# Performance work log

Hardware: AMD Instinct MI355X
Metric: run time of the kernel (lower is better)

Reference implementation:

```python
import jax, jax.numpy as jnp
import numpy as np

K = 1024   # in_dim = out_dim = per-head dim (module uses full k per head)
H = 4      # heads
B, T = 2, 2048


def setup_inputs() -> dict:
    key = jax.random.key(0)
    ks = jax.random.split(key, 7)
    s = 0.02
    return {
        "x": jax.random.normal(ks[0], (B, T, K), jnp.float32),
        "Wq": jax.random.normal(ks[1], (K, K * H), jnp.float32) * s,
        "Wk": jax.random.normal(ks[2], (K, K * H), jnp.float32) * s,
        "Wv": jax.random.normal(ks[3], (K, K * H), jnp.float32) * s,
        "Wu": jax.random.normal(ks[4], (K * H, K), jnp.float32) * s,
        "bu": jnp.zeros((K,), jnp.float32),
        "W1": jax.random.normal(ks[5], (K, K), jnp.float32) * s,
        "b1": jnp.zeros((K,), jnp.float32),
        "W2": jax.random.normal(ks[6], (K, K), jnp.float32) * s,
        "b2": jnp.zeros((K,), jnp.float32),
    }


def reference(x, Wq, Wk, Wv, Wu, bu, W1, b1, W2, b2):
    b, t, k = x.shape
    h = H
    scale = k ** (-0.25)
    # projections: each head gets FULL dim k (quirk of the original module)
    q = (x @ Wq).reshape(b, t, h, k) * scale   # [b,t,h,k]
    kk = (x @ Wk).reshape(b, t, h, k) * scale
    v = (x @ Wv).reshape(b, t, h, k)
    # attention scores [b,h,q,k_pos]
    dot = jnp.einsum("bqhd,bkhd->bhqk", q, kk)
    causal = jnp.tril(jnp.ones((t, t), bool))  # strictly-upper masked to -inf
    dot = jnp.where(causal, dot, -jnp.inf)
    attn = jax.nn.softmax(dot, axis=-1)
    out = jnp.einsum("bhqk,bkhd->bqhd", attn, v).reshape(b, t, h * k)
    attn_out = out @ Wu + bu                   # unifyheads
    x = x + attn_out                            # residual
    ff = jax.nn.relu(x @ W1 + b1) @ W2 + b2     # in_dim == out_dim
    return x + ff                               # residual around FFN
```

## Files before the change

kernel.cpp:

```cpp
#include <hip/hip_runtime.h>
#include <math.h>


#define TM 128
#define TN 128
#define BK 64

typedef __attribute__((ext_vector_type(8))) short short8;
typedef __attribute__((ext_vector_type(4))) float f32x4;

__device__ __forceinline__ unsigned short f2bf(float f) {
  union { float f; unsigned int u; } v; v.f = f;
  unsigned int r = (v.u + 0x7fffu + ((v.u >> 16) & 1u)) >> 16;
  return (unsigned short)r;
}
__device__ __forceinline__ float bf2f(unsigned short b) {
  union { unsigned int u; float f; } v; v.u = ((unsigned int)b) << 16;
  return v.f;
}

#define GL2LDS(g, l)                                                          \
  __builtin_amdgcn_global_load_lds(                                           \
      (__attribute__((address_space(1))) void*)(g),                           \
      (__attribute__((address_space(3))) void*)(l), 16, 0, 0)

__device__ __forceinline__ void gemm_core(
    const unsigned short* __restrict__ A, const unsigned short* __restrict__ BT,
    int m0, int n0, int kmax, int lda, int ldb, int ldc, long long coff,
    float scale, const float* __restrict__ bias,
    const float* __restrict__ resid, int do_relu, float* __restrict__ Cf,
    unsigned short* __restrict__ Cb, unsigned short* As, unsigned short* Bs) {
  const int tid = threadIdx.x;
  const int lane = tid & 63;
  const int wv = tid >> 6;
  const int wm = wv & 1;
  const int wn = wv >> 1;

  const int srow = tid >> 2;
  const int scol = (tid & 3) * 8;
  const unsigned short* ap0 = A + (long long)(m0 + srow) * lda + scol;
  const unsigned short* ap1 = ap0 + (long long)64 * lda;
  const unsigned short* bp0 = BT + (long long)(n0 + srow) * ldb + scol;
  const unsigned short* bp1 = bp0 + (long long)64 * ldb;
  unsigned short* lA00 = As + wv * 512;
  unsigned short* lA10 = As + 2048 + wv * 512;
  unsigned short* lA01 = As + 4096 + wv * 512;
  unsigned short* lA11 = As + 6144 + wv * 512;
  unsigned short* lB00 = Bs + wv * 512;
  unsigned short* lB10 = Bs + 2048 + wv * 512;
  unsigned short* lB01 = Bs + 4096 + wv * 512;
  unsigned short* lB11 = Bs + 6144 + wv * 512;

  f32x4 acc[4][4];
#pragma unroll
  for (int i = 0; i < 4; ++i)
#pragma unroll
    for (int j2 = 0; j2 < 4; ++j2) acc[i][j2] = {0.f, 0.f, 0.f, 0.f};

  const int frow = lane & 15;
  const int fq = (lane >> 4) * 8;

  for (int k0 = 0; k0 < kmax; k0 += BK) {
    __syncthreads();
    GL2LDS(ap0, lA00); GL2LDS(ap0 + 32, lA01);
    GL2LDS(ap1, lA10); GL2LDS(ap1 + 32, lA11);
    GL2LDS(bp0, lB00); GL2LDS(bp0 + 32, lB01);
    GL2LDS(bp1, lB10); GL2LDS(bp1 + 32, lB11);
    ap0 += BK; ap1 += BK; bp0 += BK; bp1 += BK;
    __syncthreads();

#pragma unroll
    for (int s = 0; s < 2; ++s) {
      short8 afr[4], bfr[4];
#pragma unroll
      for (int mi = 0; mi < 4; ++mi)
        afr[mi] = *(const short8*)(As + s * 4096 +
                                   (wm * 64 + mi * 16 + frow) * 32 + fq);
#pragma unroll
      for (int ni = 0; ni < 4; ++ni)
        bfr[ni] = *(const short8*)(Bs + s * 4096 +
                                   (wn * 64 + ni * 16 + frow) * 32 + fq);
#pragma unroll
      for (int mi = 0; mi < 4; ++mi)
#pragma unroll
        for (int ni = 0; ni < 4; ++ni)
          acc[mi][ni] = __builtin_amdgcn_mfma_f32_16x16x32_bf16(
              afr[mi], bfr[ni], acc[mi][ni], 0, 0, 0);
    }
  }

  const int ccol = lane & 15;
  const int crow = (lane >> 4) * 4;
#pragma unroll
  for (int mi = 0; mi < 4; ++mi) {
#pragma unroll
    for (int ni = 0; ni < 4; ++ni) {
      const int gc = n0 + wn * 64 + ni * 16 + ccol;
#pragma unroll
      for (int r = 0; r < 4; ++r) {
        const int gr = m0 + wm * 64 + mi * 16 + crow + r;
        float v = acc[mi][ni][r] * scale;
        if (bias) v += bias[gc];
        if (resid) v += resid[(long long)gr * ldc + gc];
        if (do_relu) v = fmaxf(v, 0.f);
        const long long ci = coff + (long long)gr * ldc + gc;
        if (Cf) Cf[ci] = v;
        if (Cb) Cb[ci] = f2bf(v);
      }
    }
  }
}

__device__ __forceinline__ void core64(
    f32x4 acc[4][2], const unsigned short* __restrict__ A, int lda,
    const unsigned short* __restrict__ BT, int ldb, int kmax,
    unsigned short* As, unsigned short* Bs) {
  const int tid = threadIdx.x;
  const int lane = tid & 63;
  const int wv = tid >> 6;
  const int wm = wv & 1;
  const int wn = wv >> 1;
  const int srow = tid >> 2;
  const int scol = (tid & 3) * 8;
  const unsigned short* ap0 = A + (long long)srow * lda + scol;
  const unsigned short* ap1 = ap0 + (long long)64 * lda;
  const unsigned short* bp0 = BT + (long long)srow * ldb + scol;
  unsigned short* lA00 = As + wv * 512;
  unsigned short* lA10 = As + 2048 + wv * 512;
  unsigned short* lA01 = As + 4096 + wv * 512;
  unsigned short* lA11 = As + 6144 + wv * 512;
  unsigned short* lB00 = Bs + wv * 512;
  unsigned short* lB01 = Bs + 2048 + wv * 512;
  const int frow = lane & 15;
  const int fq = (lane >> 4) * 8;
  for (int k0 = 0; k0 < kmax; k0 += 64) {
    __syncthreads();
    GL2LDS(ap0, lA00); GL2LDS(ap0 + 32, lA01);
    GL2LDS(ap1, lA10); GL2LDS(ap1 + 32, lA11);
    GL2LDS(bp0, lB00); GL2LDS(bp0 + 32, lB01);
    ap0 += 64; ap1 += 64; bp0 += 64;
    __syncthreads();
#pragma unroll
    for (int s = 0; s < 2; ++s) {
      short8 afr[4], bfr[2];
#pragma unroll
      for (int mi = 0; mi < 4; ++mi)
        afr[mi] = *(const short8*)(As + s * 4096 +
                                   (wm * 64 + mi * 16 + frow) * 32 + fq);
#pragma unroll
      for (int ni = 0; ni < 2; ++ni)
        bfr[ni] = *(const short8*)(Bs + s * 2048 +
                                   (wn * 32 + ni * 16 + frow) * 32 + fq);
#pragma unroll
      for (int mi = 0; mi < 4; ++mi)
#pragma unroll
        for (int ni = 0; ni < 2; ++ni)
          acc[mi][ni] = __builtin_amdgcn_mfma_f32_16x16x32_bf16(
              afr[mi], bfr[ni], acc[mi][ni], 0, 0, 0);
    }
  }
}

__global__ __launch_bounds__(256) void gemm_ffn(
    const unsigned short* __restrict__ A, const unsigned short* __restrict__ BT,
    const float* __restrict__ bias, const float* __restrict__ resid,
    int do_relu, float* __restrict__ Cf, unsigned short* __restrict__ Cb) {
  __shared__ unsigned short As[8192];
  __shared__ unsigned short Bs[4096];
  const int bid = blockIdx.x;
  const int xcd = bid & 7;
  const int j = bid >> 3;
  const int m0 = (xcd * 4 + (j & 3)) * 128;
  const int n0 = (j >> 2) * 64;
  f32x4 acc[4][2];
#pragma unroll
  for (int i = 0; i < 4; ++i)
#pragma unroll
    for (int j2 = 0; j2 < 2; ++j2) acc[i][j2] = {0.f, 0.f, 0.f, 0.f};
  core64(acc, A + (long long)m0 * 1024, 1024, BT + (long long)n0 * 1024, 1024,
         1024, As, Bs);
  const int lane = threadIdx.x & 63;
  const int wv = threadIdx.x >> 6;
  const int wm = wv & 1, wn = wv >> 1;
  const int ccol = lane & 15, crow = (lane >> 4) * 4;
#pragma unroll
  for (int mi = 0; mi < 4; ++mi) {
#pragma unroll
    for (int ni = 0; ni < 2; ++ni) {
      const int gc = n0 + wn * 32 + ni * 16 + ccol;
#pragma unroll
      for (int r = 0; r < 4; ++r) {
        const int gr = m0 + wm * 64 + mi * 16 + crow + r;
        float v = acc[mi][ni][r] + bias[gc];
        if (resid) v += resid[(long long)gr * 1024 + gc];
        if (do_relu) v = fmaxf(v, 0.f);
        const long long ci = (long long)gr * 1024 + gc;
        if (Cf) Cf[ci] = v;
        if (Cb) Cb[ci] = f2bf(v);
      }
    }
  }
}

__global__ __launch_bounds__(256) void gemm_bt(
    const unsigned short* __restrict__ A, const unsigned short* __restrict__ BT,
    int Kd, int lda, int ldb, int ldc, int bh_shift,
    long long aob, long long aoh, long long bob, long long boh,
    long long cob, long long coh, float scale,
    const float* __restrict__ bias, const float* __restrict__ resid,
    int do_relu, float* __restrict__ Cf, unsigned short* __restrict__ Cb,
    int causal_mode, int grid_mode) {
  __shared__ unsigned short As[8192];
  __shared__ unsigned short Bs[8192];
  int n0, m0, z;
  if (grid_mode == 2) {
    z = blockIdx.x; n0 = blockIdx.y * TN; m0 = blockIdx.z * TM;
  } else if (grid_mode == 4) {
    z = blockIdx.x; m0 = blockIdx.y * TM; n0 = blockIdx.z * TN;
  } else {
    n0 = blockIdx.x * TN; m0 = blockIdx.y * TM; z = blockIdx.z;
  }

  const int zb = z >> bh_shift;
  const int zh = z & ((1 << bh_shift) - 1);
  const long long aoff = (long long)zb * aob + (long long)zh * aoh;
  const long long boff = (long long)zb * bob + (long long)zh * boh;
  const long long coff = (long long)zb * cob + (long long)zh * coh;

  int kmax = Kd;
  if (causal_mode == 2) { int t = m0 + TM; if (t < kmax) kmax = t; }

  gemm_core(A + aoff, BT + boff, m0, n0, kmax, lda, ldb, ldc, coff, scale,
            bias, resid, do_relu, Cf, Cb, As, Bs);
}

__global__ __launch_bounds__(256) void gemm_t(
    const unsigned short* __restrict__ xb,
    const unsigned short* __restrict__ Wcomb,
    unsigned short* __restrict__ tb) {
  __shared__ unsigned short As[8192];
  __shared__ unsigned short Bs[8192];
  const int bid = blockIdx.x;
  const int xcd = bid & 7;
  const int j = bid >> 3;
  const int m0 = (xcd * 4 + (j & 3)) * TM;
  const int n0 = (j >> 2) * TN;
  gemm_core(xb, Wcomb, m0, n0, 1024, 1024, 1024, 4096, 0, 1.0f,
            nullptr, nullptr, 0, nullptr, tb, As, Bs);
}

__global__ __launch_bounds__(256) void gemm_sv(
    const unsigned short* __restrict__ xb,
    const unsigned short* __restrict__ Wcomb,
    const unsigned short* __restrict__ tb,
    unsigned short* __restrict__ S, unsigned short* __restrict__ vT) {
  __shared__ unsigned short As[8192];
  __shared__ unsigned short Bs[8192];
  const long long TT = (long long)2048 * 2048;
  const int bid = blockIdx.x;
  if (bid < 1088) {
    const int z = bid & 7, zb = z >> 2, zh = z & 3;
    const int idx = bid >> 3;
    int m = (int)((sqrtf(8.0f * idx + 1.0f) - 1.0f) * 0.5f);
    while ((m + 1) * (m + 2) / 2 <= idx) ++m;
    while (m * (m + 1) / 2 > idx) --m;
    const int m0 = m * TM;
    const int n0 = (idx - m * (m + 1) / 2) * TN;
    gemm_core(tb + (long long)zb * 2048 * 4096 + zh * 1024,
              xb + (long long)zb * 2048 * 1024,
              m0, n0, 1024, 4096, 1024, 2048,
              (long long)zb * 4 * TT + (long long)zh * TT,
              1.0f, nullptr, nullptr, 0, nullptr, S, As, Bs);
  } else {
    const int r = bid - 1088;
    const int xcd = r & 7;
    const int j = r >> 3;
    const int bb = j >> 6;
    const int rr = j & 63;
    const int m0 = (xcd * 4 + (rr & 3)) * TM;
    const int n0 = (rr >> 2) * TN;
    gemm_core(Wcomb + (size_t)4096 * 1024, xb + (long long)bb * 2048 * 1024,
              m0, n0, 1024, 1024, 1024, 2048, (long long)bb * 4096 * 2048,
              1.0f, nullptr, nullptr, 0, nullptr, vT, As, Bs);
  }
}

__global__ __launch_bounds__(256) void reduce_epi(
    const unsigned short* __restrict__ Pb, int S, long long MN,
    const float* __restrict__ bias, const float* __restrict__ resid,
    int do_relu, float* __restrict__ Cf, unsigned short* __restrict__ Cb) {
  const long long i4 = ((long long)blockIdx.x * 256 + threadIdx.x) * 4;
  if (i4 >= MN) return;
  float4 s = {0.f, 0.f, 0.f, 0.f};
  for (int t = 0; t < S; ++t) {
    const ushort4 p = *(const ushort4*)(Pb + (long long)t * MN + i4);
    s.x += bf2f(p.x); s.y += bf2f(p.y); s.z += bf2f(p.z); s.w += bf2f(p.w);
  }
  if (bias) {
    const int c0 = (int)(i4 & 1023);
    s.x += bias[c0]; s.y += bias[c0 + 1]; s.z += bias[c0 + 2]; s.w += bias[c0 + 3];
  }
  if (resid) {
    const float4 rr = *(const float4*)(resid + i4);
    s.x += rr.x; s.y += rr.y; s.z += rr.z; s.w += rr.w;
  }
  if (do_relu) {
    s.x = fmaxf(s.x, 0.f); s.y = fmaxf(s.y, 0.f);
    s.z = fmaxf(s.z, 0.f); s.w = fmaxf(s.w, 0.f);
  }
  if (Cf) *(float4*)(Cf + i4) = s;
  if (Cb) {
    ushort4 o;
    o.x = f2bf(s.x); o.y = f2bf(s.y); o.z = f2bf(s.z); o.w = f2bf(s.w);
    *(ushort4*)(Cb + i4) = o;
  }
}

__global__ __launch_bounds__(256) void softmax_causal(unsigned short* S, int T) {
  const int q = blockIdx.x;
  unsigned short* row = S + ((long long)blockIdx.y * T + q) * T;
  const int tid = threadIdx.x;
  const int lane = tid & 63;
  const int wv = tid >> 6;
  const int n = q + 1;
  const int nz = (n + 127) & ~127;
  const int base = tid * 8;
  short8 raw = {};
  if (base < nz) raw = *(const short8*)(row + base);
  float vals[8];
  float m = -__builtin_inff();
#pragma unroll
  for (int i = 0; i < 8; ++i) {
    vals[i] = (base + i < n) ? bf2f((unsigned short)raw[i]) : -__builtin_inff();
    m = fmaxf(m, vals[i]);
  }
#pragma unroll
  for (int o = 32; o; o >>= 1) m = fmaxf(m, __shfl_xor(m, o, 64));
  __shared__ float red[4];
  if (lane == 0) red[wv] = m;
  __syncthreads();
  m = fmaxf(fmaxf(red[0], red[1]), fmaxf(red[2], red[3]));
  __syncthreads();
  float s = 0.f, e[8];
#pragma unroll
  for (int i = 0; i < 8; ++i) {
    e[i] = (base + i < n) ? __expf(vals[i] - m) : 0.f;
    s += e[i];
  }
#pragma unroll
  for (int o = 32; o; o >>= 1) s += __shfl_xor(s, o, 64);
  if (lane == 0) red[wv] = s;
  __syncthreads();
  s = red[0] + red[1] + red[2] + red[3];
  const float inv = 1.f / s;
  if (base < nz) {
    short8 o8;
#pragma unroll
    for (int i = 0; i < 8; ++i) o8[i] = (short)f2bf(e[i] * inv);
    *(short8*)(row + base) = o8;
  }
}

__global__ __launch_bounds__(256) void prep_all(
    const float* __restrict__ x, const float* __restrict__ Wq,
    const float* __restrict__ Wk, const float* __restrict__ Wv,
    const float* __restrict__ Wu, const float* __restrict__ W1,
    const float* __restrict__ W2, unsigned short* __restrict__ xb,
    unsigned short* __restrict__ Wqc, unsigned short* __restrict__ Wkc,
    unsigned short* __restrict__ Wvc, unsigned short* __restrict__ WuTb,
    unsigned short* __restrict__ W1T, unsigned short* __restrict__ W2T,
    float s2) {
  const int z = blockIdx.y;
  if (z <= 3) {
    const float* src = (z == 0) ? x : (z == 1) ? Wq : (z == 2) ? Wk : Wv;
    unsigned short* dst = (z == 0) ? xb : (z == 1) ? Wqc : (z == 2) ? Wkc : Wvc;
    const float sc = (z == 2) ? s2 : 1.0f;
    const long long i4 = ((long long)blockIdx.x * 256 + threadIdx.x) * 4;
    const float4 v = *(const float4*)(src + i4);
    ushort4 u;
    u.x = f2bf(v.x * sc); u.y = f2bf(v.y * sc);
    u.z = f2bf(v.z * sc); u.w = f2bf(v.w * sc);
    *(ushort4*)(dst + i4) = u;
    return;
  }
  const int R = (z == 4) ? 4096 : 1024;
  const int by = blockIdx.x >> 5;
  if (by * 32 >= R) return;
  const float* W = (z == 4) ? Wu : (z == 5) ? W1 : W2;
  unsigned short* WT = (z == 4) ? WuTb : (z == 5) ? W1T : W2T;
  __shared__ float tile[32][33];
  const int c0 = (blockIdx.x & 31) * 32;
  const int r0 = by * 32;
  const int tx = threadIdx.x & 31;
  const int ty = threadIdx.x >> 5;
#pragma unroll
  for (int j = 0; j < 32; j += 8)
    tile[ty + j][tx] = W[(long long)(r0 + ty + j) * 1024 + c0 + tx];
  __syncthreads();
#pragma unroll
  for (int j = 0; j < 32; j += 8)
    WT[(long long)(c0 + ty + j) * R + r0 + tx] = f2bf(tile[tx][ty + j]);
}

extern "C" void kernel_launch(void* const* d_in, const int* in_sizes, int n_in,
                              void* d_out, int out_size, void* d_ws,
                              size_t ws_size, hipStream_t stream) {
  (void)in_sizes; (void)n_in; (void)out_size; (void)ws_size;
  const float* x  = (const float*)d_in[0];
  const float* Wq = (const float*)d_in[1];
  const float* Wk = (const float*)d_in[2];
  const float* Wv = (const float*)d_in[3];
  const float* Wu = (const float*)d_in[4];
  const float* bu = (const float*)d_in[5];
  const float* W1 = (const float*)d_in[6];
  const float* b1 = (const float*)d_in[7];
  const float* W2 = (const float*)d_in[8];
  const float* b2 = (const float*)d_in[9];
  float* out = (float*)d_out;

  const int T = 2048, K = 1024;
  const size_t MB = 1024 * 1024;
  const long long MN = (long long)4096 * 1024;
  const long long TT = (long long)T * T;
  const long long Mi = 1024 * 1024;

  char* w = (char*)d_ws;
  unsigned short* xb    = (unsigned short*)(w + 0 * MB);
  unsigned short* Wqc   = (unsigned short*)(w + 8 * MB);
  unsigned short* Wvc   = (unsigned short*)(w + 16 * MB);
  unsigned short* Wkc   = (unsigned short*)(w + 24 * MB);
  unsigned short* WuTb  = (unsigned short*)(w + 32 * MB);
  unsigned short* Wcomb = (unsigned short*)(w + 40 * MB);
  unsigned short* tb    = (unsigned short*)(w + 56 * MB);
  unsigned short* vT    = (unsigned short*)(w + 88 * MB);
  unsigned short* S     = (unsigned short*)(w + 120 * MB);
  unsigned short* W1T   = (unsigned short*)(w + 184 * MB);
  unsigned short* W2T   = (unsigned short*)(w + 186 * MB);
  unsigned short* Pb    = (unsigned short*)(w + 40 * MB);
  float*          x1f   = (float*)(w + 8 * MB);
  unsigned short* x1b   = (unsigned short*)(w + 24 * MB);
  unsigned short* h1    = (unsigned short*)(w + 32 * MB);

  const float s2 = 0.03125f;

  prep_all<<<dim3(4096, 7), 256, 0, stream>>>(
      x, Wq, Wk, Wv, Wu, W1, W2, xb, Wqc, Wkc, Wvc, WuTb, W1T, W2T, s2);

  gemm_bt<<<dim3(8, 8, 8), 256, 0, stream>>>(
      Wkc, Wqc, K, 4096, 4096, 1024, 2,
      4 * Mi, 1024, 4 * Mi, 1024, 4 * Mi, Mi, 1.0f,
      nullptr, nullptr, 0, nullptr, Wcomb, 0, 2);

  gemm_t<<<dim3(1024), 256, 0, stream>>>(xb, Wcomb, tb);

  gemm_sv<<<dim3(2112), 256, 0, stream>>>(xb, Wcomb, tb, S, vT);

  softmax_causal<<<dim3(T, 8), 256, 0, stream>>>(S, T);

  gemm_bt<<<dim3(8, T / TM, K / TN), 256, 0, stream>>>(
      S, vT, T, T, 2048, K, 2,
      (long long)4 * TT, TT, (long long)4096 * 2048, (long long)1024 * 2048,
      (long long)2048 * 1024, MN, 1.0f,
      nullptr, nullptr, 0, nullptr, Pb, 2, 4);

  reduce_epi<<<dim3(4096), 256, 0, stream>>>(Pb, 4, MN, bu, x, 0, x1f, x1b);

  gemm_ffn<<<dim3(512), 256, 0, stream>>>(x1b, W1T, b1, nullptr, 1,
                                          nullptr, h1);

  gemm_ffn<<<dim3(512), 256, 0, stream>>>(h1, W2T, b2, x1f, 0, out, nullptr);
}
```

Baseline: 449.8 us.

## Double-buffer LDS tiles with async prefetch and XOR swizzle in GEMM cores

Both GEMM cores (gemm_core and core64) move from a single-buffered BK=64 loop with two __syncthreads per step to a double-buffered BK=32 pipeline. The next k-slab is issued with global_load_lds while the current one is computed, using partial vmcnt waits and raw s_barrier in place of full syncs. An XOR swizzle on the global source column and the fragment read column is meant to reduce LDS bank conflicts. MFMA blocks are wrapped in s_setprio to favour issue. The cost is more barriers per unit of K and correctness that depends on the hand-tuned vmcnt counts.

```diff
diff --git a/kernel.cpp b/kernel.cpp
--- a/kernel.cpp
+++ b/kernel.cpp
@@ -4,7 +4,6 @@
 
 #define TM 128
 #define TN 128
-#define BK 64
 
 typedef __attribute__((ext_vector_type(8))) short short8;
 typedef __attribute__((ext_vector_type(4))) float f32x4;
@@ -37,19 +36,13 @@
   const int wn = wv >> 1;
 
   const int srow = tid >> 2;
-  const int scol = (tid & 3) * 8;
+  const int scol = (((tid & 3) ^ ((srow >> 1) & 3)) * 8);
   const unsigned short* ap0 = A + (long long)(m0 + srow) * lda + scol;
   const unsigned short* ap1 = ap0 + (long long)64 * lda;
   const unsigned short* bp0 = BT + (long long)(n0 + srow) * ldb + scol;
   const unsigned short* bp1 = bp0 + (long long)64 * ldb;
-  unsigned short* lA00 = As + wv * 512;
-  unsigned short* lA10 = As + 2048 + wv * 512;
-  unsigned short* lA01 = As + 4096 + wv * 512;
-  unsigned short* lA11 = As + 6144 + wv * 512;
-  unsigned short* lB00 = Bs + wv * 512;
-  unsigned short* lB10 = Bs + 2048 + wv * 512;
-  unsigned short* lB01 = Bs + 4096 + wv * 512;
-  unsigned short* lB11 = Bs + 6144 + wv * 512;
+  unsigned short* lA = As + wv * 512;
+  unsigned short* lB = Bs + wv * 512;
 
   f32x4 acc[4][4];
 #pragma unroll
@@ -58,36 +51,54 @@
     for (int j2 = 0; j2 < 4; ++j2) acc[i][j2] = {0.f, 0.f, 0.f, 0.f};
 
   const int frow = lane & 15;
-  const int fq = (lane >> 4) * 8;
-
-  for (int k0 = 0; k0 < kmax; k0 += BK) {
-    __syncthreads();
-    GL2LDS(ap0, lA00); GL2LDS(ap0 + 32, lA01);
-    GL2LDS(ap1, lA10); GL2LDS(ap1 + 32, lA11);
-    GL2LDS(bp0, lB00); GL2LDS(bp0 + 32, lB01);
-    GL2LDS(bp1, lB10); GL2LDS(bp1 + 32, lB11);
-    ap0 += BK; ap1 += BK; bp0 += BK; bp1 += BK;
-    __syncthreads();
-
-#pragma unroll
-    for (int s = 0; s < 2; ++s) {
-      short8 afr[4], bfr[4];
-#pragma unroll
-      for (int mi = 0; mi < 4; ++mi)
-        afr[mi] = *(const short8*)(As + s * 4096 +
-                                   (wm * 64 + mi * 16 + frow) * 32 + fq);
+  const int fqs = (((lane >> 4) ^ ((frow >> 1) & 3)) * 8);
+
+  int rs = 0, rc = 0;
+
+  auto stage = [&]() {
+    unsigned short* a = lA + rs * 4096;
+    unsigned short* b = lB + rs * 4096;
+    GL2LDS(ap0, a); GL2LDS(ap1, a + 2048);
+    GL2LDS(bp0, b); GL2LDS(bp1, b + 2048);
+    ap0 += 32; ap1 += 32; bp0 += 32; bp1 += 32;
+    rs ^= 1;
+  };
+  auto compute = [&]() {
+    const unsigned short* Ac = As + rc * 4096;
+    const unsigned short* Bc = Bs + rc * 4096;
+    short8 afr[4], bfr[4];
+#pragma unroll
+    for (int mi = 0; mi < 4; ++mi)
+      afr[mi] = *(const short8*)(Ac + (wm * 64 + mi * 16 + frow) * 32 + fqs);
+#pragma unroll
+    for (int ni = 0; ni < 4; ++ni)
+      bfr[ni] = *(const short8*)(Bc + (wn * 64 + ni * 16 + frow) * 32 + fqs);
+    __builtin_amdgcn_s_setprio(1);
+#pragma unroll
+    for (int mi = 0; mi < 4; ++mi)
 #pragma unroll
       for (int ni = 0; ni < 4; ++ni)
-        bfr[ni] = *(const short8*)(Bs + s * 4096 +
-                                   (wn * 64 + ni * 16 + frow) * 32 + fq);
-#pragma unroll
-      for (int mi = 0; mi < 4; ++mi)
-#pragma unroll
-        for (int ni = 0; ni < 4; ++ni)
-          acc[mi][ni] = __builtin_amdgcn_mfma_f32_16x16x32_bf16(
-              afr[mi], bfr[ni], acc[mi][ni], 0, 0, 0);
-    }
-  }
+        acc[mi][ni] = __builtin_amdgcn_mfma_f32_16x16x32_bf16(
+            afr[mi], bfr[ni], acc[mi][ni], 0, 0, 0);
+    __builtin_amdgcn_s_setprio(0);
+    rc ^= 1;
+  };
+
+  const int nsteps = kmax >> 5;
+  stage();
+  for (int i = 0; i + 1 < nsteps; ++i) {
+    stage();
+    asm volatile("s_waitcnt vmcnt(4)" ::: "memory");
+    __builtin_amdgcn_s_barrier();
+    __builtin_amdgcn_sched_barrier(0);
+    compute();
+    __builtin_amdgcn_sched_barrier(0);
+    __builtin_amdgcn_s_barrier();
+  }
+  asm volatile("s_waitcnt vmcnt(0)" ::: "memory");
+  __builtin_amdgcn_s_barrier();
+  __builtin_amdgcn_sched_barrier(0);
+  compute();
 
   const int ccol = lane & 15;
   const int crow = (lane >> 4) * 4;
@@ -121,44 +132,60 @@
   const int wm = wv & 1;
   const int wn = wv >> 1;
   const int srow = tid >> 2;
-  const int scol = (tid & 3) * 8;
+  const int scol = (((tid & 3) ^ ((srow >> 1) & 3)) * 8);
   const unsigned short* ap0 = A + (long long)srow * lda + scol;
   const unsigned short* ap1 = ap0 + (long long)64 * lda;
   const unsigned short* bp0 = BT + (long long)srow * ldb + scol;
-  unsigned short* lA00 = As + wv * 512;
-  unsigned short* lA10 = As + 2048 + wv * 512;
-  unsigned short* lA01 = As + 4096 + wv * 512;
-  unsigned short* lA11 = As + 6144 + wv * 512;
-  unsigned short* lB00 = Bs + wv * 512;
-  unsigned short* lB01 = Bs + 2048 + wv * 512;
+  unsigned short* lA = As + wv * 512;
+  unsigned short* lB = Bs + wv * 512;
   const int frow = lane & 15;
-  const int fq = (lane >> 4) * 8;
-  for (int k0 = 0; k0 < kmax; k0 += 64) {
-    __syncthreads();
-    GL2LDS(ap0, lA00); GL2LDS(ap0 + 32, lA01);
-    GL2LDS(ap1, lA10); GL2LDS(ap1 + 32, lA11);
-    GL2LDS(bp0, lB00); GL2LDS(bp0 + 32, lB01);
-    ap0 += 64; ap1 += 64; bp0 += 64;
-    __syncthreads();
-#pragma unroll
-    for (int s = 0; s < 2; ++s) {
-      short8 afr[4], bfr[2];
-#pragma unroll
-      for (int mi = 0; mi < 4; ++mi)
-        afr[mi] = *(const short8*)(As + s * 4096 +
-                                   (wm * 64 + mi * 16 + frow) * 32 + fq);
+  const int fqs = (((lane >> 4) ^ ((frow >> 1) & 3)) * 8);
+
+  int rs = 0, rc = 0;
+
+  auto stage = [&]() {
+    unsigned short* a = lA + rs * 4096;
+    GL2LDS(ap0, a); GL2LDS(ap1, a + 2048);
+    GL2LDS(bp0, lB + rs * 2048);
+    ap0 += 32; ap1 += 32; bp0 += 32;
+    rs ^= 1;
+  };
+  auto compute = [&]() {
+    const unsigned short* Ac = As + rc * 4096;
+    const unsigned short* Bc = Bs + rc * 2048;
+    short8 afr[4], bfr[2];
+#pragma unroll
+    for (int mi = 0; mi < 4; ++mi)
+      afr[mi] = *(const short8*)(Ac + (wm * 64 + mi * 16 + frow) * 32 + fqs);
+#pragma unroll
+    for (int ni = 0; ni < 2; ++ni)
+      bfr[ni] = *(const short8*)(Bc + (wn * 32 + ni * 16 + frow) * 32 + fqs);
+    __builtin_amdgcn_s_setprio(1);
+#pragma unroll
+    for (int mi = 0; mi < 4; ++mi)
 #pragma unroll
       for (int ni = 0; ni < 2; ++ni)
-        bfr[ni] = *(const short8*)(Bs + s * 2048 +
-                                   (wn * 32 + ni * 16 + frow) * 32 + fq);
-#pragma unroll
-      for (int mi = 0; mi < 4; ++mi)
-#pragma unroll
-        for (int ni = 0; ni < 2; ++ni)
-          acc[mi][ni] = __builtin_amdgcn_mfma_f32_16x16x32_bf16(
-              afr[mi], bfr[ni], acc[mi][ni], 0, 0, 0);
-    }
-  }
+        acc[mi][ni] = __builtin_amdgcn_mfma_f32_16x16x32_bf16(
+            afr[mi], bfr[ni], acc[mi][ni], 0, 0, 0);
+    __builtin_amdgcn_s_setprio(0);
+    rc ^= 1;
+  };
+
+  const int nsteps = kmax >> 5;
+  stage();
+  for (int i = 0; i + 1 < nsteps; ++i) {
+    stage();
+    asm volatile("s_waitcnt vmcnt(3)" ::: "memory");
+    __builtin_amdgcn_s_barrier();
+    __builtin_amdgcn_sched_barrier(0);
+    compute();
+    __builtin_amdgcn_sched_barrier(0);
+    __builtin_amdgcn_s_barrier();
+  }
+  asm volatile("s_waitcnt vmcnt(0)" ::: "memory");
+  __builtin_amdgcn_s_barrier();
+  __builtin_amdgcn_sched_barrier(0);
+  compute();
 }
 
 __global__ __launch_bounds__(256) void gemm_ffn(
```

After: 441.8 us. Within noise of the previous version (-1.8%).
